# Performance work log

Measured on AMD Instinct MI355X. Metric: run time of the kernel, lower is better.

The kernel has to match this reference:

```python
import jax, jax.numpy as jnp
import numpy as np

N = 50000   # nodes
E = 640000  # edges
D_IN = 128
D_OUT = 128
EPS = 1e-5


def _layer_norm(x, gamma, beta):
    mu = jnp.mean(x, axis=-1, keepdims=True)
    var = jnp.mean(jnp.square(x - mu), axis=-1, keepdims=True)
    return (x - mu) * jax.lax.rsqrt(var + EPS) * gamma + beta


def _sage_conv(x, src, dst, w_l, b_l, w_r):
    # PyG SAGEConv (aggr='mean', root_weight=True, normalize=False):
    #   out = lin_l(mean_{j in N(i)} x_j) + lin_r(x_i)
    msgs = x[src]                                             # [E, D]
    agg = jax.ops.segment_sum(msgs, dst, num_segments=N)      # [N, D]
    cnt = jax.ops.segment_sum(jnp.ones((E,), x.dtype), dst, num_segments=N)
    mean = agg / jnp.maximum(cnt, 1.0)[:, None]
    return mean @ w_l.T + b_l + x @ w_r.T


def setup_inputs() -> dict:
    key = jax.random.key(0)
    ks = jax.random.split(key, 12)
    s_in = 1.0 / np.sqrt(D_IN)
    s_out = 1.0 / np.sqrt(D_OUT)
    return {
        "x": jax.random.normal(ks[0], (N, D_IN), jnp.float32),
        "edges": jax.random.randint(ks[1], (2, E), 0, N),
        "dp_w": jax.random.uniform(ks[2], (D_OUT, D_IN), jnp.float32, -s_in, s_in),
        "dp_b": jnp.zeros((D_OUT,), jnp.float32),
        "sc_w": jax.random.uniform(ks[3], (D_OUT, D_IN), jnp.float32, -s_in, s_in),
        "sc_b": jnp.zeros((D_OUT,), jnp.float32),
        "g1_lw": jax.random.uniform(ks[4], (D_OUT, D_OUT), jnp.float32, -s_out, s_out),
        "g1_lb": jnp.zeros((D_OUT,), jnp.float32),
        "g1_rw": jax.random.uniform(ks[5], (D_OUT, D_OUT), jnp.float32, -s_out, s_out),
        "n1_g": jnp.ones((D_OUT,), jnp.float32),
        "n1_b": jnp.zeros((D_OUT,), jnp.float32),
        "g2_lw": jax.random.uniform(ks[6], (D_OUT, D_OUT), jnp.float32, -s_out, s_out),
        "g2_lb": jnp.zeros((D_OUT,), jnp.float32),
        "g2_rw": jax.random.uniform(ks[7], (D_OUT, D_OUT), jnp.float32, -s_out, s_out),
        "n2_g": jnp.ones((D_OUT,), jnp.float32),
        "n2_b": jnp.zeros((D_OUT,), jnp.float32),
    }


def reference(x, edges, dp_w, dp_b, sc_w, sc_b, g1_lw, g1_lb, g1_rw, n1_g, n1_b,
              g2_lw, g2_lb, g2_rw, n2_g, n2_b):
    gelu = lambda v: jax.nn.gelu(v, approximate=False)
    src, dst = edges[0], edges[1]
    shortcut = x @ sc_w.T + sc_b
    h = gelu(x @ dp_w.T + dp_b)
    h = _sage_conv(h, src, dst, g1_lw, g1_lb, g1_rw)
    h = gelu(_layer_norm(h, n1_g, n1_b))
    h = _sage_conv(h, src, dst, g2_lw, g2_lb, g2_rw)
    h = _layer_norm(h, n2_g, n2_b)
    return gelu(h + shortcut)
```

## Files before the change

### kernel.cpp

```cpp
#include <hip/hip_runtime.h>
#include <hip/hip_bf16.h>
#include <math.h>

#define D 128
#define WS 136
#define FS 132
#define PB 128

typedef __attribute__((ext_vector_type(8))) short bf16x8;
typedef __attribute__((ext_vector_type(4))) float f32x4;

__device__ __forceinline__ unsigned short f2bf(float f){
  return (unsigned short)((__float_as_uint(f) + 0x8000u) >> 16);
}
__device__ __forceinline__ float bf2f(unsigned short h){
  return __uint_as_float(((unsigned)h) << 16);
}
__device__ __forceinline__ float bf2f_lo(unsigned v){
  return __uint_as_float(v << 16);
}
__device__ __forceinline__ float bf2f_hi(unsigned v){
  return __uint_as_float(v & 0xFFFF0000u);
}
__device__ __forceinline__ float gelu_fast(float v){
  float u = v * v;
  float arg = v * (1.5957691216f + 0.0713548163f * u);
  arg = fminf(arg, 60.0f);
  float e = __expf(arg);
  return v * e * __builtin_amdgcn_rcpf(e + 1.0f);
}

__global__ __launch_bounds__(256) void k_prepcnt(const float* s0, const float* s1,
    const float* s2, const float* s3, const float* s4, const float* s5,
    unsigned short* dst, const int* __restrict__ edst, int* __restrict__ cnt,
    int E, int nbuck, int epb){
  __shared__ int hist[512];
  if (blockIdx.x < 48){
    int gt = blockIdx.x * 256 + threadIdx.x;
    int m = gt >> 11;
    int r = gt & 2047;
    int f = r >> 6, lane = r & 63;
    int t = f & 7, kk = f >> 3;
    int row = t * 16 + (lane & 15);
    int col = kk * 32 + (lane >> 4) * 8;
    const float* src;
    if (m == 0) src = s0; else if (m == 1) src = s1; else if (m == 2) src = s2;
    else if (m == 3) src = s3; else if (m == 4) src = s4; else src = s5;
    src += row * 128 + col;
    float4 a = *(const float4*)src;
    float4 bb = *(const float4*)(src + 4);
    bf16x8 o;
    o[0] = (short)f2bf(a.x);  o[1] = (short)f2bf(a.y);
    o[2] = (short)f2bf(a.z);  o[3] = (short)f2bf(a.w);
    o[4] = (short)f2bf(bb.x); o[5] = (short)f2bf(bb.y);
    o[6] = (short)f2bf(bb.z); o[7] = (short)f2bf(bb.w);
    int pair = m >> 1, half = m & 1;
    *(bf16x8*)(dst + (size_t)pair * 32768 + (((size_t)f * 2 + half) * 64 + lane) * 8) = o;
    return;
  }
  int blk = blockIdx.x - 48;
  for (int b = threadIdx.x; b < nbuck; b += 256) hist[b] = 0;
  __syncthreads();
  int start = blk * epb;
  int end = min(E, start + epb);
  for (int e = start + threadIdx.x; e < end; e += 256)
    atomicAdd(&hist[edst[e] >> 7], 1);
  __syncthreads();
  for (int b = threadIdx.x; b < nbuck; b += 256) cnt[blk * nbuck + b] = hist[b];
}

__global__ __launch_bounds__(128) void k_scanA(const int* __restrict__ cnt,
    int* __restrict__ offs_rel, int* __restrict__ tot, int nbuck){
  __shared__ int sm[128];
  int b = blockIdx.x, t = threadIdx.x;
  int v = cnt[t * nbuck + b];
  sm[t] = v; __syncthreads();
  for (int ofs = 1; ofs < 128; ofs <<= 1){
    int u = (t >= ofs) ? sm[t - ofs] : 0;
    __syncthreads();
    sm[t] += u;
    __syncthreads();
  }
  offs_rel[t * nbuck + b] = sm[t] - v;
  if (t == 127) tot[b] = sm[127];
}

__global__ __launch_bounds__(256) void k_pscatter(const int* __restrict__ esrc,
    const int* __restrict__ edst, const int* __restrict__ offs_rel,
    const int* __restrict__ tot, unsigned* __restrict__ ebuf,
    int E, int nbuck, int epb){
  __shared__ int stot[512];
  __shared__ int loff[512];
  for (int b = threadIdx.x; b < nbuck; b += 256) stot[b] = tot[b];
  __syncthreads();
  for (int b = threadIdx.x; b < nbuck; b += 256){
    int s = 0;
    for (int j = 0; j < b; j++) s += stot[j];
    loff[b] = s + offs_rel[blockIdx.x * nbuck + b];
  }
  __syncthreads();
  int start = blockIdx.x * epb;
  int end = min(E, start + epb);
  for (int e = start + threadIdx.x; e < end; e += 256){
    int s = esrc[e], d = edst[e];
    int b = d >> 7;
    int pos = atomicAdd(&loff[b], 1);
    ebuf[pos] = (unsigned)s | ((unsigned)(d & 127) << 16);
  }
}

__global__ __launch_bounds__(256) void k_csrin(
    const unsigned* __restrict__ ebuf, const int* __restrict__ tot,
    int* __restrict__ off, int* __restrict__ csr,
    const float* __restrict__ x, const unsigned short* __restrict__ wp,
    const float* __restrict__ scb, const float* __restrict__ dpb,
    unsigned short* __restrict__ sbuf, unsigned short* __restrict__ hbuf,
    int N, int E, int nbuck){
  __shared__ int cnt[128], pref[128], curs[128];
  __shared__ int stot[512], red[256];
  __shared__ unsigned short tile[64 * WS];
  int tid = threadIdx.x;
  if ((int)blockIdx.x < nbuck){
    int b = blockIdx.x;
    for (int j = tid; j < nbuck; j += 256) stot[j] = tot[j];
    __syncthreads();
    int part = 0;
    for (int j = tid; j < b; j += 256) part += stot[j];
    red[tid] = part;
    __syncthreads();
    for (int ofs = 128; ofs > 0; ofs >>= 1){
      if (tid < ofs) red[tid] += red[tid + ofs];
      __syncthreads();
    }
    int start = red[0];
    int end = start + stot[b];
    if (tid < 128) cnt[tid] = 0;
    __syncthreads();
    for (int e = start + tid; e < end; e += 256)
      atomicAdd(&cnt[ebuf[e] >> 16], 1);
    __syncthreads();
    if (tid < 128) pref[tid] = cnt[tid];
    __syncthreads();
    for (int ofs = 1; ofs < 128; ofs <<= 1){
      int v = 0;
      if (tid < 128 && tid >= ofs) v = pref[tid - ofs];
      __syncthreads();
      if (tid < 128) pref[tid] += v;
      __syncthreads();
    }
    if (tid < 128){
      int ex = pref[tid] - cnt[tid];
      curs[tid] = ex;
      int node = b * 128 + tid;
      if (node < N) off[node] = start + ex;
    }
    if (b == 0 && tid == 0) off[N] = E;
    __syncthreads();
    for (int e = start + tid; e < end; e += 256){
      unsigned u = ebuf[e];
      int d = u >> 16;
      int p = atomicAdd(&curs[d], 1);
      csr[start + p] = (int)(u & 0xFFFFu);
    }
    return;
  }
  int bx = blockIdx.x - nbuck;
  int w = tid >> 6, lane = tid & 63, quad = lane >> 4, l16 = lane & 15;
  int nbb = bx * 64;
  int nb = nbb + w * 16;
  int arow = min(nb + l16, N - 1);
  f32x4 acc[2][8];
  #pragma unroll
  for (int m = 0; m < 2; m++)
    #pragma unroll
    for (int t = 0; t < 8; t++) acc[m][t] = (f32x4){0.f, 0.f, 0.f, 0.f};
  #pragma unroll
  for (int kk = 0; kk < 4; kk++){
    const float* xp = x + (size_t)arow * D + kk * 32 + quad * 8;
    float4 xa = *(const float4*)xp;
    float4 xb = *(const float4*)(xp + 4);
    bf16x8 a;
    a[0] = (short)f2bf(xa.x); a[1] = (short)f2bf(xa.y);
    a[2] = (short)f2bf(xa.z); a[3] = (short)f2bf(xa.w);
    a[4] = (short)f2bf(xb.x); a[5] = (short)f2bf(xb.y);
    a[6] = (short)f2bf(xb.z); a[7] = (short)f2bf(xb.w);
    #pragma unroll
    for (int t = 0; t < 8; t++){
      size_t fo = (((size_t)(kk * 8 + t) * 2) * 64 + lane) * 8;
      bf16x8 b0 = *(const bf16x8*)(wp + fo);
      bf16x8 b1 = *(const bf16x8*)(wp + fo + 512);
      acc[0][t] = __builtin_amdgcn_mfma_f32_16x16x32_bf16(a, b0, acc[0][t], 0, 0, 0);
      acc[1][t] = __builtin_amdgcn_mfma_f32_16x16x32_bf16(a, b1, acc[1][t], 0, 0, 0);
    }
  }
  #pragma unroll
  for (int m = 0; m < 2; m++){
    const float* bias = m ? dpb : scb;
    #pragma unroll
    for (int t = 0; t < 8; t++){
      float bv = bias[t * 16 + l16];
      #pragma unroll
      for (int r = 0; r < 4; r++){
        int nl = w * 16 + quad * 4 + r;
        float v = acc[m][t][r] + bv;
        if (m) v = gelu_fast(v);
        tile[nl * WS + t * 16 + l16] = f2bf(v);
      }
    }
    __syncthreads();
    unsigned short* dst = m ? hbuf : sbuf;
    #pragma unroll
    for (int i = 0; i < 4; i++){
      int c = tid + 256 * i;
      int nl = c >> 4, j = c & 15;
      int node = nbb + nl;
      if (node < N)
        *(bf16x8*)(dst + (size_t)node * D + j * 8) = *(const bf16x8*)(tile + nl * WS + j * 8);
    }
    __syncthreads();
  }
}

__global__ __launch_bounds__(256) void k_layer(
    const unsigned short* __restrict__ hin,
    const int* __restrict__ off, const int* __restrict__ csr,
    const unsigned short* __restrict__ wp,
    const float* __restrict__ lb, const float* __restrict__ gamma,
    const float* __restrict__ beta,
    const unsigned short* __restrict__ sbuf,
    unsigned short* __restrict__ hout, float* __restrict__ fout, int N, int mode){
  extern __shared__ char smraw[];
  unsigned short* mtile = (unsigned short*)smraw;
  unsigned short* stile = (unsigned short*)smraw;
  float* ftile = (float*)smraw;
  int tid = threadIdx.x;
  int nbb = blockIdx.x * 64;
  {
    int g = tid >> 4, l16g = tid & 15;
    const unsigned short* hp = hin + l16g * 8;
    #pragma unroll
    for (int pass = 0; pass < 4; pass++){
      int nl = pass * 16 + g;
      int nodec = min(nbb + nl, N - 1);
      int s0 = off[nodec], s1 = off[nodec + 1];
      float acc[8];
      #pragma unroll
      for (int c = 0; c < 8; c++) acc[c] = 0.f;
      if (s1 > s0){
        int nn[8];
        #pragma unroll
        for (int i = 0; i < 8; i++) nn[i] = csr[min(s0 + i, s1 - 1)];
        for (int e = s0; e < s1; e += 8){
          uint4 v[8];
          #pragma unroll
          for (int i = 0; i < 8; i++)
            v[i] = *(const uint4*)(hp + (size_t)nn[i] * D);
          #pragma unroll
          for (int i = 0; i < 8; i++) nn[i] = csr[min(e + 8 + i, s1 - 1)];
          #pragma unroll
          for (int i = 0; i < 8; i++){
            float m = (e + i < s1) ? 1.f : 0.f;
            acc[0] += m * bf2f_lo(v[i].x);
            acc[1] += m * bf2f_hi(v[i].x);
            acc[2] += m * bf2f_lo(v[i].y);
            acc[3] += m * bf2f_hi(v[i].y);
            acc[4] += m * bf2f_lo(v[i].z);
            acc[5] += m * bf2f_hi(v[i].z);
            acc[6] += m * bf2f_lo(v[i].w);
            acc[7] += m * bf2f_hi(v[i].w);
          }
        }
      }
      float inv = 1.f / (float)max(s1 - s0, 1);
      bf16x8 o;
      #pragma unroll
      for (int c = 0; c < 8; c++) o[c] = (short)f2bf(acc[c] * inv);
      *(bf16x8*)(mtile + nl * WS + l16g * 8) = o;
    }
  }
  __syncthreads();
  int w = tid >> 6, lane = tid & 63, quad = lane >> 4, l16 = lane & 15;
  int nb = nbb + w * 16;
  int arow = min(nb + l16, N - 1);
  int mrow = w * 16 + l16;
  bf16x8 am[4], ah[4];
  #pragma unroll
  for (int kk = 0; kk < 4; kk++){
    am[kk] = *(const bf16x8*)(mtile + mrow * WS + kk * 32 + quad * 8);
    ah[kk] = *(const bf16x8*)(hin + (size_t)arow * D + kk * 32 + quad * 8);
  }
  f32x4 acc[8];
  #pragma unroll
  for (int t = 0; t < 8; t++) acc[t] = (f32x4){0.f, 0.f, 0.f, 0.f};
  #pragma unroll
  for (int kk = 0; kk < 4; kk++){
    #pragma unroll
    for (int t = 0; t < 8; t++){
      size_t fo = (((size_t)(kk * 8 + t) * 2) * 64 + lane) * 8;
      bf16x8 bl = *(const bf16x8*)(wp + fo);
      bf16x8 br = *(const bf16x8*)(wp + fo + 512);
      acc[t] = __builtin_amdgcn_mfma_f32_16x16x32_bf16(am[kk], bl, acc[t], 0, 0, 0);
      acc[t] = __builtin_amdgcn_mfma_f32_16x16x32_bf16(ah[kk], br, acc[t], 0, 0, 0);
    }
  }
  float lbv[8], gv[8], bv[8];
  #pragma unroll
  for (int t = 0; t < 8; t++){
    lbv[t] = lb[t * 16 + l16];
    gv[t] = gamma[t * 16 + l16];
    bv[t] = beta[t * 16 + l16];
  }
  float mu[4], rs[4];
  #pragma unroll
  for (int r = 0; r < 4; r++){
    float s = 0.f, qq = 0.f;
    #pragma unroll
    for (int t = 0; t < 8; t++){
      float v = acc[t][r] + lbv[t];
      acc[t][r] = v;
      s += v; qq += v * v;
    }
    s += __shfl_xor(s, 1); qq += __shfl_xor(qq, 1);
    s += __shfl_xor(s, 2); qq += __shfl_xor(qq, 2);
    s += __shfl_xor(s, 4); qq += __shfl_xor(qq, 4);
    s += __shfl_xor(s, 8); qq += __shfl_xor(qq, 8);
    float m_ = s * (1.f / 128.f);
    mu[r] = m_;
    rs[r] = rsqrtf(qq * (1.f / 128.f) - m_ * m_ + 1e-5f);
  }
  __syncthreads();
  if (mode == 0){
    #pragma unroll
    for (int t = 0; t < 8; t++)
      #pragma unroll
      for (int r = 0; r < 4; r++){
        int nl = w * 16 + quad * 4 + r;
        float v = (acc[t][r] - mu[r]) * rs[r] * gv[t] + bv[t];
        stile[nl * WS + t * 16 + l16] = f2bf(gelu_fast(v));
      }
    __syncthreads();
    #pragma unroll
    for (int i = 0; i < 4; i++){
      int c = tid + 256 * i;
      int nl = c >> 4, j = c & 15;
      int node = nbb + nl;
      if (node < N)
        *(bf16x8*)(hout + (size_t)node * D + j * 8) = *(const bf16x8*)(stile + nl * WS + j * 8);
    }
  } else {
    #pragma unroll
    for (int i = 0; i < 4; i++){
      int c = tid + 256 * i;
      int nl = c >> 4, j = c & 15;
      int node = nbb + nl;
      bf16x8 v = (bf16x8){0,0,0,0,0,0,0,0};
      if (node < N) v = *(const bf16x8*)(sbuf + (size_t)node * D + j * 8);
      *(bf16x8*)(stile + nl * WS + j * 8) = v;
    }
    __syncthreads();
    float sc[8][4];
    #pragma unroll
    for (int t = 0; t < 8; t++)
      #pragma unroll
      for (int r = 0; r < 4; r++){
        int nl = w * 16 + quad * 4 + r;
        sc[t][r] = bf2f(stile[nl * WS + t * 16 + l16]);
      }
    __syncthreads();
    #pragma unroll
    for (int t = 0; t < 8; t++)
      #pragma unroll
      for (int r = 0; r < 4; r++){
        int nl = w * 16 + quad * 4 + r;
        float v = (acc[t][r] - mu[r]) * rs[r] * gv[t] + bv[t];
        ftile[nl * FS + t * 16 + l16] = gelu_fast(v + sc[t][r]);
      }
    __syncthreads();
    #pragma unroll
    for (int i = 0; i < 8; i++){
      int c = tid + 256 * i;
      int nl = c >> 5, j = c & 31;
      int node = nbb + nl;
      if (node < N)
        *(float4*)(fout + (size_t)node * D + j * 4) = *(const float4*)(ftile + nl * FS + j * 4);
    }
  }
}

extern "C" void kernel_launch(void* const* d_in, const int* in_sizes, int n_in,
                              void* d_out, int out_size, void* d_ws, size_t ws_size,
                              hipStream_t stream){
  const float* x     = (const float*)d_in[0];
  const int*   edges = (const int*)d_in[1];
  const float* dp_w  = (const float*)d_in[2];
  const float* dp_b  = (const float*)d_in[3];
  const float* sc_w  = (const float*)d_in[4];
  const float* sc_b  = (const float*)d_in[5];
  const float* g1_lw = (const float*)d_in[6];
  const float* g1_lb = (const float*)d_in[7];
  const float* g1_rw = (const float*)d_in[8];
  const float* n1_g  = (const float*)d_in[9];
  const float* n1_b  = (const float*)d_in[10];
  const float* g2_lw = (const float*)d_in[11];
  const float* g2_lb = (const float*)d_in[12];
  const float* g2_rw = (const float*)d_in[13];
  const float* n2_g  = (const float*)d_in[14];
  const float* n2_b  = (const float*)d_in[15];

  const int N = in_sizes[0] / D;
  const int E = in_sizes[1] / 2;
  const int* esrc = edges;
  const int* edst = edges + E;
  const int nbuck = (N + 127) >> 7;
  const int epb = (E + PB - 1) / PB;

  char* base = (char*)d_ws;
  size_t cur = 0;
  auto carve = [&](size_t b) -> char* {
    char* p = base + cur;
    cur = (cur + b + 255) & ~(size_t)255;
    return p;
  };
  unsigned* ebuf  = (unsigned*)carve((size_t)E * 4);
  int* cnt        = (int*)carve((size_t)PB * nbuck * 4);
  int* offs_rel   = (int*)carve((size_t)PB * nbuck * 4);
  int* tot        = (int*)carve((size_t)nbuck * 4);
  int* off        = (int*)carve((size_t)(N + 1) * 4);
  int* csr        = (int*)carve((size_t)E * 4);
  unsigned short* wb    = (unsigned short*)carve((size_t)3 * 32768 * 2);
  unsigned short* hbuf  = (unsigned short*)carve((size_t)N * D * 2);
  unsigned short* h1buf = (unsigned short*)carve((size_t)N * D * 2);
  unsigned short* sbuf  = (unsigned short*)carve((size_t)N * D * 2);

  unsigned short* wp0 = wb;
  unsigned short* wp1 = wb + 32768;
  unsigned short* wp2 = wb + 2 * 32768;

  float* out = (float*)d_out;

  k_prepcnt<<<48 + PB, 256, 0, stream>>>(sc_w, dp_w, g1_lw, g1_rw, g2_lw, g2_rw,
                                         wb, edst, cnt, E, nbuck, epb);
  k_scanA<<<nbuck, 128, 0, stream>>>(cnt, offs_rel, tot, nbuck);
  k_pscatter<<<PB, 256, 0, stream>>>(esrc, edst, offs_rel, tot, ebuf, E, nbuck, epb);

  const int nin = (N + 63) / 64;
  k_csrin<<<nbuck + nin, 256, 0, stream>>>(ebuf, tot, off, csr,
                                           x, wp0, sc_b, dp_b, sbuf, hbuf,
                                           N, E, nbuck);

  k_layer<<<nin, 256, 17408, stream>>>(hbuf, off, csr, wp1, g1_lb, n1_g, n1_b,
                                       nullptr, h1buf, nullptr, N, 0);
  k_layer<<<nin, 256, 33792, stream>>>(h1buf, off, csr, wp2, g2_lb, n2_g, n2_b,
                                       sbuf, nullptr, out, N, 1);
}
```

Before: 233.0 us.

## Make layer kernel wave-independent with per-wave LDS tiles, drop block barriers

Each wave now owns its own 16-node tile end to end. It gathers neighbor means into a private LDS slice, runs the MFMA GEMM, the layernorm and the epilogue on that slice, and writes out, so all __syncthreads calls become wave-local lgkmcnt waits. This removes block-wide barrier stalls that arise when waves see unequal neighbor counts, and lets waves proceed independently. The change relies on intra-wave LDS ordering being enforced by s_waitcnt plus a sched_barrier. Early return of out-of-range waves is safe only because no block barriers remain.

```diff
diff --git a/kernel.cpp b/kernel.cpp
--- a/kernel.cpp
+++ b/kernel.cpp
@@ -28,6 +28,10 @@
   arg = fminf(arg, 60.0f);
   float e = __expf(arg);
   return v * e * __builtin_amdgcn_rcpf(e + 1.0f);
+}
+__device__ __forceinline__ void lds_fence(){
+  asm volatile("s_waitcnt lgkmcnt(0)" ::: "memory");
+  __builtin_amdgcn_sched_barrier(0);
 }
 
 __global__ __launch_bounds__(256) void k_prepcnt(const float* s0, const float* s1,
@@ -228,20 +232,26 @@
     const float* __restrict__ lb, const float* __restrict__ gamma,
     const float* __restrict__ beta,
     const unsigned short* __restrict__ sbuf,
-    unsigned short* __restrict__ hout, float* __restrict__ fout, int N, int mode){
+    unsigned short* __restrict__ hout, float* __restrict__ fout,
+    int N, int ntiles, int mode){
   extern __shared__ char smraw[];
-  unsigned short* mtile = (unsigned short*)smraw;
-  unsigned short* stile = (unsigned short*)smraw;
-  float* ftile = (float*)smraw;
   int tid = threadIdx.x;
-  int nbb = blockIdx.x * 64;
+  int w = tid >> 6, lane = tid & 63;
+  int quad = lane >> 4, l16 = lane & 15;
+  int tix = blockIdx.x * 4 + w;
+  if (tix >= ntiles) return;
+  int nbb = tix * 16;
+  int pw = mode ? (16 * FS * 4) : (16 * WS * 2);
+  char* wbase = smraw + (size_t)w * pw;
+  unsigned short* mtile = (unsigned short*)wbase;
+  unsigned short* stile = (unsigned short*)wbase;
+  float* ftile = (float*)wbase;
   {
-    int g = tid >> 4, l16g = tid & 15;
-    const unsigned short* hp = hin + l16g * 8;
-    #pragma unroll
-    for (int pass = 0; pass < 4; pass++){
-      int nl = pass * 16 + g;
-      int nodec = min(nbb + nl, N - 1);
+    const unsigned short* hp = hin + l16 * 8;
+    #pragma unroll
+    for (int p = 0; p < 4; p++){
+      int r = p * 4 + quad;
+      int nodec = min(nbb + r, N - 1);
       int s0 = off[nodec], s1 = off[nodec + 1];
       float acc[8];
       #pragma unroll
@@ -275,18 +285,15 @@
       bf16x8 o;
       #pragma unroll
       for (int c = 0; c < 8; c++) o[c] = (short)f2bf(acc[c] * inv);
-      *(bf16x8*)(mtile + nl * WS + l16g * 8) = o;
-    }
-  }
-  __syncthreads();
-  int w = tid >> 6, lane = tid & 63, quad = lane >> 4, l16 = lane & 15;
-  int nb = nbb + w * 16;
-  int arow = min(nb + l16, N - 1);
-  int mrow = w * 16 + l16;
+      *(bf16x8*)(mtile + r * WS + l16 * 8) = o;
+    }
+  }
+  lds_fence();
+  int arow = min(nbb + l16, N - 1);
   bf16x8 am[4], ah[4];
   #pragma unroll
   for (int kk = 0; kk < 4; kk++){
-    am[kk] = *(const bf16x8*)(mtile + mrow * WS + kk * 32 + quad * 8);
+    am[kk] = *(const bf16x8*)(mtile + l16 * WS + kk * 32 + quad * 8);
     ah[kk] = *(const bf16x8*)(hin + (size_t)arow * D + kk * 32 + quad * 8);
   }
   f32x4 acc[8];
@@ -328,20 +335,20 @@
     mu[r] = m_;
     rs[r] = rsqrtf(qq * (1.f / 128.f) - m_ * m_ + 1e-5f);
   }
-  __syncthreads();
+  lds_fence();
   if (mode == 0){
     #pragma unroll
     for (int t = 0; t < 8; t++)
       #pragma unroll
       for (int r = 0; r < 4; r++){
-        int nl = w * 16 + quad * 4 + r;
+        int nl = quad * 4 + r;
         float v = (acc[t][r] - mu[r]) * rs[r] * gv[t] + bv[t];
         stile[nl * WS + t * 16 + l16] = f2bf(gelu_fast(v));
       }
-    __syncthreads();
+    lds_fence();
     #pragma unroll
     for (int i = 0; i < 4; i++){
-      int c = tid + 256 * i;
+      int c = lane + 64 * i;
       int nl = c >> 4, j = c & 15;
       int node = nbb + nl;
       if (node < N)
@@ -350,35 +357,35 @@
   } else {
     #pragma unroll
     for (int i = 0; i < 4; i++){
-      int c = tid + 256 * i;
+      int c = lane + 64 * i;
       int nl = c >> 4, j = c & 15;
       int node = nbb + nl;
       bf16x8 v = (bf16x8){0,0,0,0,0,0,0,0};
       if (node < N) v = *(const bf16x8*)(sbuf + (size_t)node * D + j * 8);
       *(bf16x8*)(stile + nl * WS + j * 8) = v;
     }
-    __syncthreads();
+    lds_fence();
     float sc[8][4];
     #pragma unroll
     for (int t = 0; t < 8; t++)
       #pragma unroll
       for (int r = 0; r < 4; r++){
-        int nl = w * 16 + quad * 4 + r;
+        int nl = quad * 4 + r;
         sc[t][r] = bf2f(stile[nl * WS + t * 16 + l16]);
       }
-    __syncthreads();
+    lds_fence();
     #pragma unroll
     for (int t = 0; t < 8; t++)
       #pragma unroll
       for (int r = 0; r < 4; r++){
-        int nl = w * 16 + quad * 4 + r;
+        int nl = quad * 4 + r;
         float v = (acc[t][r] - mu[r]) * rs[r] * gv[t] + bv[t];
         ftile[nl * FS + t * 16 + l16] = gelu_fast(v + sc[t][r]);
       }
-    __syncthreads();
+    lds_fence();
     #pragma unroll
     for (int i = 0; i < 8; i++){
-      int c = tid + 256 * i;
+      int c = lane + 64 * i;
       int nl = c >> 5, j = c & 31;
       int node = nbb + nl;
       if (node < N)
@@ -448,8 +455,10 @@
                                            x, wp0, sc_b, dp_b, sbuf, hbuf,
                                            N, E, nbuck);
 
-  k_layer<<<nin, 256, 17408, stream>>>(hbuf, off, csr, wp1, g1_lb, n1_g, n1_b,
-                                       nullptr, h1buf, nullptr, N, 0);
-  k_layer<<<nin, 256, 33792, stream>>>(h1buf, off, csr, wp2, g2_lb, n2_g, n2_b,
-                                       sbuf, nullptr, out, N, 1);
-}
+  const int ntiles = (N + 15) >> 4;
+  const int ngrid = (ntiles + 3) >> 2;
+  k_layer<<<ngrid, 256, 17408, stream>>>(hbuf, off, csr, wp1, g1_lb, n1_g, n1_b,
+                                         nullptr, h1buf, nullptr, N, ntiles, 0);
+  k_layer<<<ngrid, 256, 33792, stream>>>(h1buf, off, csr, wp2, g2_lb, n2_g, n2_b,
+                                         sbuf, nullptr, out, N, ntiles, 1);
+}
```

Result: slower. 243.6 us (+4.5%).

## Gather neighbor features from an FP8 copy to halve aggregation traffic

Applied to the files above, without the earlier changes.

Producers of the hidden features now also write an FP8 (e4m3) copy of each row next to the bf16 one. The mean-aggregation gather in each SAGE layer reads 16 FP8 values per 16-byte load instead of 8 bf16 values, so each neighbor row costs half the bytes. Thread mapping changes to 8 lanes per node and 2 passes to match. The cost is an extra FP8 write per row and reduced precision in the aggregated messages, which may hurt accuracy tolerance.

```diff
diff --git a/kernel.cpp b/kernel.cpp
--- a/kernel.cpp
+++ b/kernel.cpp
@@ -9,6 +9,7 @@
 
 typedef __attribute__((ext_vector_type(8))) short bf16x8;
 typedef __attribute__((ext_vector_type(4))) float f32x4;
+typedef __attribute__((ext_vector_type(2))) float f32x2;
 
 __device__ __forceinline__ unsigned short f2bf(float f){
   return (unsigned short)((__float_as_uint(f) + 0x8000u) >> 16);
@@ -28,6 +29,13 @@
   arg = fminf(arg, 60.0f);
   float e = __expf(arg);
   return v * e * __builtin_amdgcn_rcpf(e + 1.0f);
+}
+__device__ __forceinline__ uint2 pack_fp8_8(const float* f){
+  int a = __builtin_amdgcn_cvt_pk_fp8_f32(f[0], f[1], 0, false);
+  a = __builtin_amdgcn_cvt_pk_fp8_f32(f[2], f[3], a, true);
+  int b = __builtin_amdgcn_cvt_pk_fp8_f32(f[4], f[5], 0, false);
+  b = __builtin_amdgcn_cvt_pk_fp8_f32(f[6], f[7], b, true);
+  return make_uint2((unsigned)a, (unsigned)b);
 }
 
 __global__ __launch_bounds__(256) void k_prepcnt(const float* s0, const float* s1,
@@ -115,6 +123,7 @@
     const float* __restrict__ x, const unsigned short* __restrict__ wp,
     const float* __restrict__ scb, const float* __restrict__ dpb,
     unsigned short* __restrict__ sbuf, unsigned short* __restrict__ hbuf,
+    unsigned char* __restrict__ hb8,
     int N, int E, int nbuck){
   __shared__ int cnt[128], pref[128], curs[128];
   __shared__ int stot[512], red[256];
@@ -214,8 +223,16 @@
       int c = tid + 256 * i;
       int nl = c >> 4, j = c & 15;
       int node = nbb + nl;
-      if (node < N)
-        *(bf16x8*)(dst + (size_t)node * D + j * 8) = *(const bf16x8*)(tile + nl * WS + j * 8);
+      if (node < N){
+        bf16x8 t8 = *(const bf16x8*)(tile + nl * WS + j * 8);
+        *(bf16x8*)(dst + (size_t)node * D + j * 8) = t8;
+        if (m){
+          float f[8];
+          #pragma unroll
+          for (int q = 0; q < 8; q++) f[q] = bf2f((unsigned short)t8[q]);
+          *(uint2*)(hb8 + (size_t)node * 128 + j * 8) = pack_fp8_8(f);
+        }
+      }
     }
     __syncthreads();
   }
@@ -223,12 +240,14 @@
 
 __global__ __launch_bounds__(256) void k_layer(
     const unsigned short* __restrict__ hin,
+    const unsigned char* __restrict__ gin8,
     const int* __restrict__ off, const int* __restrict__ csr,
     const unsigned short* __restrict__ wp,
     const float* __restrict__ lb, const float* __restrict__ gamma,
     const float* __restrict__ beta,
     const unsigned short* __restrict__ sbuf,
-    unsigned short* __restrict__ hout, float* __restrict__ fout, int N, int mode){
+    unsigned short* __restrict__ hout, unsigned char* __restrict__ hout8,
+    float* __restrict__ fout, int N, int mode){
   extern __shared__ char smraw[];
   unsigned short* mtile = (unsigned short*)smraw;
   unsigned short* stile = (unsigned short*)smraw;
@@ -236,16 +255,16 @@
   int tid = threadIdx.x;
   int nbb = blockIdx.x * 64;
   {
-    int g = tid >> 4, l16g = tid & 15;
-    const unsigned short* hp = hin + l16g * 8;
-    #pragma unroll
-    for (int pass = 0; pass < 4; pass++){
-      int nl = pass * 16 + g;
+    int g = tid >> 3, l8 = tid & 7;
+    const unsigned char* hp8 = gin8 + (size_t)l8 * 16;
+    #pragma unroll
+    for (int pass = 0; pass < 2; pass++){
+      int nl = pass * 32 + g;
       int nodec = min(nbb + nl, N - 1);
       int s0 = off[nodec], s1 = off[nodec + 1];
-      float acc[8];
-      #pragma unroll
-      for (int c = 0; c < 8; c++) acc[c] = 0.f;
+      float acc[16];
+      #pragma unroll
+      for (int c = 0; c < 16; c++) acc[c] = 0.f;
       if (s1 > s0){
         int nn[8];
         #pragma unroll
@@ -254,28 +273,40 @@
           uint4 v[8];
           #pragma unroll
           for (int i = 0; i < 8; i++)
-            v[i] = *(const uint4*)(hp + (size_t)nn[i] * D);
+            v[i] = *(const uint4*)(hp8 + (size_t)nn[i] * 128);
           #pragma unroll
           for (int i = 0; i < 8; i++) nn[i] = csr[min(e + 8 + i, s1 - 1)];
           #pragma unroll
           for (int i = 0; i < 8; i++){
             float m = (e + i < s1) ? 1.f : 0.f;
-            acc[0] += m * bf2f_lo(v[i].x);
-            acc[1] += m * bf2f_hi(v[i].x);
-            acc[2] += m * bf2f_lo(v[i].y);
-            acc[3] += m * bf2f_hi(v[i].y);
-            acc[4] += m * bf2f_lo(v[i].z);
-            acc[5] += m * bf2f_hi(v[i].z);
-            acc[6] += m * bf2f_lo(v[i].w);
-            acc[7] += m * bf2f_hi(v[i].w);
+            f32x2 p0 = __builtin_amdgcn_cvt_pk_f32_fp8((int)v[i].x, false);
+            f32x2 p1 = __builtin_amdgcn_cvt_pk_f32_fp8((int)v[i].x, true);
+            f32x2 p2 = __builtin_amdgcn_cvt_pk_f32_fp8((int)v[i].y, false);
+            f32x2 p3 = __builtin_amdgcn_cvt_pk_f32_fp8((int)v[i].y, true);
+            f32x2 p4 = __builtin_amdgcn_cvt_pk_f32_fp8((int)v[i].z, false);
+            f32x2 p5 = __builtin_amdgcn_cvt_pk_f32_fp8((int)v[i].z, true);
+            f32x2 p6 = __builtin_amdgcn_cvt_pk_f32_fp8((int)v[i].w, false);
+            f32x2 p7 = __builtin_amdgcn_cvt_pk_f32_fp8((int)v[i].w, true);
+            acc[0]  = fmaf(m, p0.x, acc[0]);  acc[1]  = fmaf(m, p0.y, acc[1]);
+            acc[2]  = fmaf(m, p1.x, acc[2]);  acc[3]  = fmaf(m, p1.y, acc[3]);
+            acc[4]  = fmaf(m, p2.x, acc[4]);  acc[5]  = fmaf(m, p2.y, acc[5]);
+            acc[6]  = fmaf(m, p3.x, acc[6]);  acc[7]  = fmaf(m, p3.y, acc[7]);
+            acc[8]  = fmaf(m, p4.x, acc[8]);  acc[9]  = fmaf(m, p4.y, acc[9]);
+            acc[10] = fmaf(m, p5.x, acc[10]); acc[11] = fmaf(m, p5.y, acc[11]);
+            acc[12] = fmaf(m, p6.x, acc[12]); acc[13] = fmaf(m, p6.y, acc[13]);
+            acc[14] = fmaf(m, p7.x, acc[14]); acc[15] = fmaf(m, p7.y, acc[15]);
           }
         }
       }
       float inv = 1.f / (float)max(s1 - s0, 1);
-      bf16x8 o;
-      #pragma unroll
-      for (int c = 0; c < 8; c++) o[c] = (short)f2bf(acc[c] * inv);
-      *(bf16x8*)(mtile + nl * WS + l16g * 8) = o;
+      bf16x8 o0, o1;
+      #pragma unroll
+      for (int c = 0; c < 8; c++){
+        o0[c] = (short)f2bf(acc[c] * inv);
+        o1[c] = (short)f2bf(acc[8 + c] * inv);
+      }
+      *(bf16x8*)(mtile + nl * WS + l8 * 16) = o0;
+      *(bf16x8*)(mtile + nl * WS + l8 * 16 + 8) = o1;
     }
   }
   __syncthreads();
@@ -344,8 +375,14 @@
       int c = tid + 256 * i;
       int nl = c >> 4, j = c & 15;
       int node = nbb + nl;
-      if (node < N)
-        *(bf16x8*)(hout + (size_t)node * D + j * 8) = *(const bf16x8*)(stile + nl * WS + j * 8);
+      if (node < N){
+        bf16x8 t8 = *(const bf16x8*)(stile + nl * WS + j * 8);
+        *(bf16x8*)(hout + (size_t)node * D + j * 8) = t8;
+        float f[8];
+        #pragma unroll
+        for (int q = 0; q < 8; q++) f[q] = bf2f((unsigned short)t8[q]);
+        *(uint2*)(hout8 + (size_t)node * 128 + j * 8) = pack_fp8_8(f);
+      }
     }
   } else {
     #pragma unroll
@@ -431,6 +468,8 @@
   unsigned short* hbuf  = (unsigned short*)carve((size_t)N * D * 2);
   unsigned short* h1buf = (unsigned short*)carve((size_t)N * D * 2);
   unsigned short* sbuf  = (unsigned short*)carve((size_t)N * D * 2);
+  unsigned char*  hbuf8  = (unsigned char*)carve((size_t)N * 128);
+  unsigned char*  h1buf8 = (unsigned char*)carve((size_t)N * 128);
 
   unsigned short* wp0 = wb;
   unsigned short* wp1 = wb + 32768;
@@ -445,11 +484,11 @@
 
   const int nin = (N + 63) / 64;
   k_csrin<<<nbuck + nin, 256, 0, stream>>>(ebuf, tot, off, csr,
-                                           x, wp0, sc_b, dp_b, sbuf, hbuf,
+                                           x, wp0, sc_b, dp_b, sbuf, hbuf, hbuf8,
                                            N, E, nbuck);
 
-  k_layer<<<nin, 256, 17408, stream>>>(hbuf, off, csr, wp1, g1_lb, n1_g, n1_b,
-                                       nullptr, h1buf, nullptr, N, 0);
-  k_layer<<<nin, 256, 33792, stream>>>(h1buf, off, csr, wp2, g2_lb, n2_g, n2_b,
-                                       sbuf, nullptr, out, N, 1);
-}
+  k_layer<<<nin, 256, 17408, stream>>>(hbuf, hbuf8, off, csr, wp1, g1_lb, n1_g, n1_b,
+                                       nullptr, h1buf, h1buf8, nullptr, N, 0);
+  k_layer<<<nin, 256, 33792, stream>>>(h1buf, h1buf8, off, csr, wp2, g2_lb, n2_g, n2_b,
+                                       sbuf, nullptr, nullptr, out, N, 1);
+}
```

Result: faster. 228.0 us, median of 2 (-2.2%).
